# Kernel optimization log

Measured on AMD Instinct MI355X. Metric: run time of the kernel, lower is better.

The kernel has to match this reference:

```python
import jax, jax.numpy as jnp
import numpy as np

BETA = 0.95
THR = 1.0
NUM_STEPS = 25
NUM_IN, NUM_HID, NUM_OUT = 9, 100, 2
BATCH = 65536


def _heaviside(x):
    return (x > 0).astype(x.dtype)


def setup_inputs() -> dict:
    key = jax.random.key(0)
    ks = jax.random.split(key, 5)
    x = jax.random.normal(ks[0], (BATCH, NUM_IN), dtype=jnp.float32)
    # nn.Linear default init: U(-1/sqrt(fan_in), 1/sqrt(fan_in))
    b1lim = 1.0 / np.sqrt(NUM_IN)
    b2lim = 1.0 / np.sqrt(NUM_HID)
    W1 = jax.random.uniform(ks[1], (NUM_HID, NUM_IN), jnp.float32, -b1lim, b1lim)
    b1 = jax.random.uniform(ks[2], (NUM_HID,), jnp.float32, -b1lim, b1lim)
    W2 = jax.random.uniform(ks[3], (NUM_OUT, NUM_HID), jnp.float32, -b2lim, b2lim)
    b2 = jax.random.uniform(ks[4], (NUM_OUT,), jnp.float32, -b2lim, b2lim)
    return {"x": x, "W1": W1, "b1": b1, "W2": W2, "b2": b2}


def reference(x, W1, b1, W2, b2):
    # cur1 = fc1(x) is identical every step (x is static) -> hoist out of loop
    cur1 = x @ W1.T + b1                     # [B, 100]
    mem1 = jnp.zeros((x.shape[0], NUM_HID), x.dtype)
    mem2 = jnp.zeros((x.shape[0], NUM_OUT), x.dtype)

    def step(carry, _):
        mem1, mem2 = carry
        # snntorch Leaky, reset_mechanism='subtract': reset from PREVIOUS mem
        reset1 = _heaviside(mem1 - THR)
        mem1 = BETA * mem1 + cur1 - reset1 * THR
        spk1 = _heaviside(mem1 - THR)        # [B, 100]
        cur2 = spk1 @ W2.T + b2              # [B, 2]
        reset2 = _heaviside(mem2 - THR)
        mem2 = BETA * mem2 + cur2 - reset2 * THR
        return (mem1, mem2), mem2

    (_, _), mem2_rec = jax.lax.scan(step, (mem1, mem2), None, length=NUM_STEPS)
    return mem2_rec                          # [25, B, 2]
```

## Files before the change

kernel.cpp:

```cpp
#include <hip/hip_runtime.h>

#define BATCH  65536
#define NIN    9
#define NHID   100
#define TSTEPS 25
#define CHUNK  5
#define EPS    5e-5f

typedef float v2f __attribute__((ext_vector_type(2)));

__global__ __launch_bounds__(256) void snn_kernel(
    const float* __restrict__ x,  const float* __restrict__ W1,
    const float* __restrict__ b1, const float* __restrict__ W2,
    const float* __restrict__ b2, float* __restrict__ out)
{
    __shared__ float sx[64 * NIN];
    __shared__ v2f   sacc[2][4][CHUNK][64];

    const int tid  = threadIdx.x;
    const int lane = tid & 63;
    const int wq   = __builtin_amdgcn_readfirstlane(tid >> 6);
    const int b0   = blockIdx.x * 64;

    for (int i = tid; i < 64 * NIN; i += 256) sx[i] = x[(size_t)b0 * NIN + i];
    __syncthreads();

    float xv[NIN];
#pragma unroll
    for (int i = 0; i < NIN; ++i) xv[i] = sx[lane * NIN + i];

    v2f acc[TSTEPS];
#pragma unroll
    for (int t = 0; t < TSTEPS; ++t) acc[t] = (v2f){0.f, 0.f};

    const int h0 = wq * 25;
#pragma unroll 1
    for (int j = 0; j < 25; ++j) {
        const int h = h0 + j;
        float c32 = 0.f;
#pragma unroll
        for (int i = 0; i < NIN; ++i) c32 = fmaf(W1[h * NIN + i], xv[i], c32);
        c32 += b1[h];
        const float c1_32 = c32 - 1.0f;
        const float w0 = W2[h], w1 = W2[NHID + h];
        const v2f   w  = (v2f){w0, w1};

        float m = 0.f, ming = 1e30f;
        bool  s = false;
#pragma unroll
        for (int t = 0; t < TSTEPS; ++t) {
            float cs = s ? c1_32 : c32;
            m = fmaf(0.95f, m, cs);
            float g = m - 1.0f;
            s = (g > 0.0f);
            ming = fminf(ming, fabsf(g));
            float d = s ? 1.f : 0.f;
            acc[t] += (v2f){d, d} * w;
        }

        if (__any(ming < EPS)) {
            double c64 = 0.0;
#pragma unroll
            for (int i = 0; i < NIN; ++i)
                c64 += (double)W1[h * NIN + i] * (double)xv[i];
            c64 += (double)b1[h];
            const double c1_64 = c64 - 1.0;

            double md = 0.0;  bool sd = false;
            float  mr = 0.f;  bool sr = false;
#pragma unroll
            for (int t = 0; t < TSTEPS; ++t) {
                float csr = sr ? c1_32 : c32;
                mr = fmaf(0.95f, mr, csr);
                sr = ((mr - 1.0f) > 0.0f);
                md = 0.95 * md + (sd ? c1_64 : c64);
                sd = (md > 1.0);
                if (sr != sd) {
                    float sg = sd ? 1.f : -1.f;
                    acc[t] += (v2f){sg, sg} * w;
                }
            }
        }
    }

    double m20 = 0.0, m21 = 0.0;
    double bb0 = (double)b2[0], bb1 = (double)b2[1];

#pragma unroll
    for (int k = 0; k < TSTEPS / CHUNK; ++k) {
#pragma unroll
        for (int u = 0; u < CHUNK; ++u)
            sacc[k & 1][wq][u][lane] = acc[k * CHUNK + u];
        __syncthreads();
        if (wq == 0) {
#pragma unroll
            for (int u = 0; u < CHUNK; ++u) {
                const int t = k * CHUNK + u;
                v2f q0 = sacc[k & 1][0][u][lane];
                v2f q1 = sacc[k & 1][1][u][lane];
                v2f q2 = sacc[k & 1][2][u][lane];
                v2f q3 = sacc[k & 1][3][u][lane];
                v2f sum = (q0 + q1) + (q2 + q3);
                double r0 = (m20 > 1.0) ? 1.0 : 0.0;
                double r1 = (m21 > 1.0) ? 1.0 : 0.0;
                m20 = 0.95 * m20 + ((double)sum[0] + bb0) - r0;
                m21 = 0.95 * m21 + ((double)sum[1] + bb1) - r1;
                *(float2*)(out + ((size_t)t * BATCH + b0 + lane) * 2) =
                    make_float2((float)m20, (float)m21);
            }
        }
    }
}

extern "C" void kernel_launch(void* const* d_in, const int* in_sizes, int n_in,
                              void* d_out, int out_size, void* d_ws, size_t ws_size,
                              hipStream_t stream) {
    const float* x  = (const float*)d_in[0];
    const float* W1 = (const float*)d_in[1];
    const float* b1 = (const float*)d_in[2];
    const float* W2 = (const float*)d_in[3];
    const float* b2 = (const float*)d_in[4];
    float* out = (float*)d_out;

    dim3 grid(BATCH / 64), block(256);
    hipLaunchKernelGGL(snn_kernel, grid, block, 0, stream, x, W1, b1, W2, b2, out);
}
```

Baseline: 102.3 us.

## Encode hidden spike trains as bitmasks and accumulate fc2 after the loop

```diff
diff --git a/kernel.cpp b/kernel.cpp
--- a/kernel.cpp
+++ b/kernel.cpp
@@ -5,7 +5,7 @@
 #define NHID   100
 #define TSTEPS 25
 #define CHUNK  5
-#define EPS    5e-5f
+#define EPS    3e-5f
 
 typedef float v2f __attribute__((ext_vector_type(2)));
 
@@ -14,8 +14,9 @@
     const float* __restrict__ b1, const float* __restrict__ W2,
     const float* __restrict__ b2, float* __restrict__ out)
 {
-    __shared__ float sx[64 * NIN];
-    __shared__ v2f   sacc[2][4][CHUNK][64];
+    __shared__ float    sx[64 * NIN];
+    __shared__ unsigned smsk[4][25][64];
+    __shared__ v2f      sacc[2][4][CHUNK][64];
 
     const int tid  = threadIdx.x;
     const int lane = tid & 63;
@@ -29,11 +30,8 @@
 #pragma unroll
     for (int i = 0; i < NIN; ++i) xv[i] = sx[lane * NIN + i];
 
-    v2f acc[TSTEPS];
-#pragma unroll
-    for (int t = 0; t < TSTEPS; ++t) acc[t] = (v2f){0.f, 0.f};
+    const int h0 = wq * 25;
 
-    const int h0 = wq * 25;
 #pragma unroll 1
     for (int j = 0; j < 25; ++j) {
         const int h = h0 + j;
@@ -41,21 +39,19 @@
 #pragma unroll
         for (int i = 0; i < NIN; ++i) c32 = fmaf(W1[h * NIN + i], xv[i], c32);
         c32 += b1[h];
-        const float c1_32 = c32 - 1.0f;
-        const float w0 = W2[h], w1 = W2[NHID + h];
-        const v2f   w  = (v2f){w0, w1};
+        const float k  = c32 - 0.05f;
+        const float k1 = c32 - 1.05f;
 
-        float m = 0.f, ming = 1e30f;
+        float u = -1.0f, ming = 1e30f, ma = 0.f, mb = 0.f;
         bool  s = false;
 #pragma unroll
         for (int t = 0; t < TSTEPS; ++t) {
-            float cs = s ? c1_32 : c32;
-            m = fmaf(0.95f, m, cs);
-            float g = m - 1.0f;
-            s = (g > 0.0f);
-            ming = fminf(ming, fabsf(g));
+            u = fmaf(0.95f, u, s ? k1 : k);
+            s = (u > 0.0f);
+            ming = fminf(ming, fabsf(u));
             float d = s ? 1.f : 0.f;
-            acc[t] += (v2f){d, d} * w;
+            if (t < 13) ma = fmaf(d, (float)(1u << t),        ma);
+            else        mb = fmaf(d, (float)(1u << (t - 13)), mb);
         }
 
         if (__any(ming < EPS)) {
@@ -64,42 +60,58 @@
             for (int i = 0; i < NIN; ++i)
                 c64 += (double)W1[h * NIN + i] * (double)xv[i];
             c64 += (double)b1[h];
-            const double c1_64 = c64 - 1.0;
-
+            const double c1 = c64 - 1.0;
             double md = 0.0;  bool sd = false;
-            float  mr = 0.f;  bool sr = false;
+            ma = 0.f;  mb = 0.f;
 #pragma unroll
             for (int t = 0; t < TSTEPS; ++t) {
-                float csr = sr ? c1_32 : c32;
-                mr = fmaf(0.95f, mr, csr);
-                sr = ((mr - 1.0f) > 0.0f);
-                md = 0.95 * md + (sd ? c1_64 : c64);
+                md = 0.95 * md + (sd ? c1 : c64);
                 sd = (md > 1.0);
-                if (sr != sd) {
-                    float sg = sd ? 1.f : -1.f;
-                    acc[t] += (v2f){sg, sg} * w;
-                }
+                float d = sd ? 1.f : 0.f;
+                if (t < 13) ma = fmaf(d, (float)(1u << t),        ma);
+                else        mb = fmaf(d, (float)(1u << (t - 13)), mb);
             }
         }
+        smsk[wq][j][lane] = (unsigned)ma | ((unsigned)mb << 13);
     }
+
+    float w0s[25], w1s[25];
+#pragma unroll
+    for (int j = 0; j < 25; ++j) {
+        w0s[j] = W2[h0 + j];
+        w1s[j] = W2[NHID + h0 + j];
+    }
+
+    unsigned mr[25];
+#pragma unroll
+    for (int j = 0; j < 25; ++j) mr[j] = smsk[wq][j][lane];
 
     double m20 = 0.0, m21 = 0.0;
     double bb0 = (double)b2[0], bb1 = (double)b2[1];
 
 #pragma unroll
-    for (int k = 0; k < TSTEPS / CHUNK; ++k) {
+    for (int kc = 0; kc < TSTEPS / CHUNK; ++kc) {
 #pragma unroll
-        for (int u = 0; u < CHUNK; ++u)
-            sacc[k & 1][wq][u][lane] = acc[k * CHUNK + u];
+        for (int uu = 0; uu < CHUNK; ++uu) {
+            const int t = kc * CHUNK + uu;
+            float a0 = 0.f, a1 = 0.f;
+#pragma unroll
+            for (int j = 0; j < 25; ++j) {
+                float d = (float)((mr[j] >> t) & 1u);
+                a0 = fmaf(d, w0s[j], a0);
+                a1 = fmaf(d, w1s[j], a1);
+            }
+            sacc[kc & 1][wq][uu][lane] = (v2f){a0, a1};
+        }
         __syncthreads();
         if (wq == 0) {
 #pragma unroll
-            for (int u = 0; u < CHUNK; ++u) {
-                const int t = k * CHUNK + u;
-                v2f q0 = sacc[k & 1][0][u][lane];
-                v2f q1 = sacc[k & 1][1][u][lane];
-                v2f q2 = sacc[k & 1][2][u][lane];
-                v2f q3 = sacc[k & 1][3][u][lane];
+            for (int uu = 0; uu < CHUNK; ++uu) {
+                const int t = kc * CHUNK + uu;
+                v2f q0 = sacc[kc & 1][0][uu][lane];
+                v2f q1 = sacc[kc & 1][1][uu][lane];
+                v2f q2 = sacc[kc & 1][2][uu][lane];
+                v2f q3 = sacc[kc & 1][3][uu][lane];
                 v2f sum = (q0 + q1) + (q2 + q3);
                 double r0 = (m20 > 1.0) ? 1.0 : 0.0;
                 double r1 = (m21 > 1.0) ? 1.0 : 0.0;
```

Result: slower. 108.5 us (+6.1%).
